# Performance work log

Hardware: AMD Instinct MI355X
Metric: run time of the kernel (lower is better)

## Reference

```python
import jax, jax.numpy as jnp
import numpy as np

WS = 7       # window_size
SHIFT = 3    # shift_size
NH = 4       # num_heads


def _layernorm(x, g, b, eps=1e-5):
    m = jnp.mean(x, axis=-1, keepdims=True)
    v = jnp.mean((x - m) ** 2, axis=-1, keepdims=True)
    return (x - m) * jax.lax.rsqrt(v + eps) * g + b


def _mha(x, wq, bq, wk, bk, wv, bv, wo, bo):
    # x: [n, s, c]; weights stored as [in, out]
    n, s, c = x.shape
    dk = c // NH
    q = (x @ wq + bq).reshape(n, s, NH, dk).transpose(0, 2, 1, 3)
    k = (x @ wk + bk).reshape(n, s, NH, dk).transpose(0, 2, 1, 3)
    v = (x @ wv + bv).reshape(n, s, NH, dk).transpose(0, 2, 1, 3)
    scores = jnp.einsum('nhqd,nhkd->nhqk', q, k) / jnp.sqrt(jnp.float32(dk))
    attn = jax.nn.softmax(scores, axis=-1)  # dropout is identity in eval
    out = jnp.einsum('nhqk,nhkd->nhqd', attn, v)
    out = out.transpose(0, 2, 1, 3).reshape(n, s, c)
    return out @ wo + bo


def _window_partition(x):
    B, H, W, C = x.shape
    x = x.reshape(B, H // WS, WS, W // WS, WS, C)
    x = x.transpose(0, 1, 3, 2, 4, 5)
    return x.reshape(-1, WS * WS, C)


def _window_reverse(wins, H, W):
    C = wins.shape[-1]
    B = wins.shape[0] // ((H // WS) * (W // WS))
    x = wins.reshape(B, H // WS, W // WS, WS, WS, C)
    x = x.transpose(0, 1, 3, 2, 4, 5)
    return x.reshape(B, H, W, C)


def setup_inputs() -> dict:
    key = jax.random.key(0)
    ks = jax.random.split(key, 16)
    C = 128
    def w(k, shape):
        return jax.random.normal(k, shape, dtype=jnp.float32) * 0.02
    return {
        'x':  jax.random.normal(ks[0], (4, 56, 56, C), dtype=jnp.float32),
        'wq': w(ks[1], (C, C)), 'bq': jnp.zeros((C,), jnp.float32),
        'wk': w(ks[2], (C, C)), 'bk': jnp.zeros((C,), jnp.float32),
        'wv': w(ks[3], (C, C)), 'bv': jnp.zeros((C,), jnp.float32),
        'wo': w(ks[4], (C, C)), 'bo': jnp.zeros((C,), jnp.float32),
        'w1': w(ks[5], (C, 4 * C)), 'b1': jnp.zeros((4 * C,), jnp.float32),
        'w2': w(ks[6], (4 * C, C)), 'b2': jnp.zeros((C,), jnp.float32),
        'g1': jnp.ones((C,), jnp.float32), 'be1': jnp.zeros((C,), jnp.float32),
        'g2': jnp.ones((C,), jnp.float32), 'be2': jnp.zeros((C,), jnp.float32),
    }


def reference(x, wq, bq, wk, bk, wv, bv, wo, bo, w1, b1, w2, b2, g1, be1, g2, be2):
    B, H, W, C = x.shape
    # cyclic shift
    xs = jnp.roll(x, shift=(-SHIFT, -SHIFT), axis=(1, 2)) if SHIFT > 0 else x
    # windowed attention (note: original code replaces x, no residual here)
    wins = _window_partition(xs)                         # [B*nW, 49, C]
    attn_wins = _mha(wins, wq, bq, wk, bk, wv, bv, wo, bo)
    xs = _window_reverse(attn_wins, H, W)
    x = jnp.roll(xs, shift=(SHIFT, SHIFT), axis=(1, 2)) if SHIFT > 0 else xs
    # global attention residual branch (flatten H*W tokens)
    xf = x.reshape(B, H * W, C)
    xf = xf + _mha(_layernorm(xf, g1, be1), wq, bq, wk, bk, wv, bv, wo, bo)
    # MLP residual branch
    h = jax.nn.gelu(_layernorm(xf, g2, be2) @ w1 + b1, approximate=False)
    xf = xf + (h @ w2 + b2)
    return xf.reshape(B, H, W, C)
```

## Files before the change

kernel.cpp:

```cpp
#include <hip/hip_runtime.h>
#include <hip/hip_bf16.h>
#include <math.h>

#define NH 4
#define DK 32
#define CC 128
#define HW 56
#define SHIFT 3
#define NTOK 12544
#define S_GLB 3136
#define VTW_STRIDE 12608
#define SCALE_L2E 0.25503488f

typedef unsigned short u16;
typedef short bf16x8 __attribute__((ext_vector_type(8)));
typedef unsigned short u16x8 __attribute__((ext_vector_type(8)));
typedef float f32x4 __attribute__((ext_vector_type(4)));

static __device__ __forceinline__ u16 f2bf(float f) {
  unsigned int b = __builtin_bit_cast(unsigned int, f);
  return (u16)((b + 0x7FFFu + ((b >> 16) & 1u)) >> 16);
}
static __device__ __forceinline__ unsigned pk2bf(float a, float b) {
  unsigned r;
  asm("v_cvt_pk_bf16_f32 %0, %1, %2" : "=v"(r) : "v"(a), "v"(b));
  return r;
}
static __device__ __forceinline__ float fexp2(float x) {
  float r;
  asm("v_exp_f32 %0, %1" : "=v"(r) : "v"(x));
  return r;
}
static __device__ __forceinline__ void gload16(const void* g, void* l) {
  __builtin_amdgcn_global_load_lds(
      (const __attribute__((address_space(1))) unsigned int*)g,
      (__attribute__((address_space(3))) unsigned int*)l, 16, 0, 0);
}

__global__ __launch_bounds__(256) void prep_k(
    const float* __restrict__ w1, const float* __restrict__ w2,
    const float* __restrict__ wq, const float* __restrict__ wk,
    const float* __restrict__ wv, const float* __restrict__ wo,
    const float* __restrict__ x,
    u16* __restrict__ w1t, u16* __restrict__ w2t,
    u16* __restrict__ wqkvt, u16* __restrict__ wot, u16* __restrict__ xg) {
  if (blockIdx.x < 768) {
    const int idx = blockIdx.x * 256 + threadIdx.x;
    if (idx < 65536) {
      const int c = idx >> 7, r = idx & 127;
      w1t[idx] = f2bf(w1[r * 512 + c]);
    } else if (idx < 131072) {
      const int o = idx - 65536;
      const int c = o / 512, r = o - c * 512;
      w2t[o] = f2bf(w2[r * 128 + c]);
    } else {
      const int o = idx - 131072;
      const int which = o >> 14, oo = o & 16383;
      const int c = oo >> 7, r = oo & 127;
      const float* src = (which == 0) ? wq : (which == 1) ? wk : (which == 2) ? wv : wo;
      u16* dst = (which < 3) ? (wqkvt + which * 16384) : wot;
      dst[oo] = f2bf(src[r * 128 + c]);
    }
  } else {
    const int bid = blockIdx.x - 768;
    const int t = bid * 2 + (threadIdx.x >> 7);
    const int c = threadIdx.x & 127;
    const int win = t / 49, tok = t % 49;
    const int b = win >> 6, wrem = win & 63;
    const int wi = wrem >> 3, wj = wrem & 7;
    const int i = tok / 7, j = tok % 7;
    int hh = wi * 7 + i + SHIFT; if (hh >= HW) hh -= HW;
    int ww = wj * 7 + j + SHIFT; if (ww >= HW) ww -= HW;
    xg[(size_t)t * CC + c] = f2bf(x[((size_t)(b * HW + hh) * HW + ww) * CC + c]);
  }
}

template <int PATH>
__global__ __launch_bounds__(256) void qkv_gemm_k(
    const u16* __restrict__ xin, const u16* __restrict__ wqkvt,
    const float* __restrict__ bq, const float* __restrict__ bk,
    const float* __restrict__ bv,
    u16* __restrict__ qo, u16* __restrict__ ko, u16* __restrict__ vto) {
  __shared__ __align__(16) u16 xs[64][136];
  __shared__ __align__(16) u16 wt[64][136];
  const int tid = threadIdx.x;
  const int w = tid >> 6, lane = tid & 63;
  const int lo = lane & 15, hi = lane >> 4, hi4 = hi * 4;
  const int m0 = blockIdx.x * 64;
  const int widx = blockIdx.y >> 1;
  const int n0 = (blockIdx.y & 1) * 64;
  {
    const int r = tid >> 2, sg = tid & 3;
    const u16* sx = &xin[(size_t)(m0 + r) * CC + sg * 32];
    const u16* sw = &wqkvt[(size_t)widx * CC * CC + (size_t)(n0 + r) * CC + sg * 32];
#pragma unroll
    for (int j = 0; j < 4; ++j) {
      *reinterpret_cast<u16x8*>(&xs[r][sg * 32 + j * 8]) = *reinterpret_cast<const u16x8*>(&sx[j * 8]);
      *reinterpret_cast<u16x8*>(&wt[r][sg * 32 + j * 8]) = *reinterpret_cast<const u16x8*>(&sw[j * 8]);
    }
  }
  __syncthreads();
  if (widx < 2) {
    const float* bias = (widx == 0) ? bq : bk;
    u16* outp = (widx == 0) ? qo : ko;
    const float oscale = (widx == 0) ? SCALE_L2E : 1.0f;
    f32x4 acc[4];
#pragma unroll
    for (int st = 0; st < 4; ++st) {
      const float b_ = bias[n0 + st * 16 + lo];
      acc[st] = (f32x4){b_, b_, b_, b_};
    }
#pragma unroll
    for (int kk = 0; kk < 4; ++kk) {
      const bf16x8 af = *reinterpret_cast<const bf16x8*>(&xs[w * 16 + lo][kk * 32 + 8 * hi]);
#pragma unroll
      for (int st = 0; st < 4; ++st) {
        const bf16x8 bfr = *reinterpret_cast<const bf16x8*>(&wt[st * 16 + lo][kk * 32 + 8 * hi]);
        acc[st] = __builtin_amdgcn_mfma_f32_16x16x32_bf16(af, bfr, acc[st], 0, 0, 0);
      }
    }
#pragma unroll
    for (int r = 0; r < 4; ++r) {
      const int mm = m0 + w * 16 + hi4 + r;
      size_t rowbase, hstride;
      if (PATH == 0) {
        const int win = mm / 49, tok = mm - win * 49;
        rowbase = ((size_t)(win * 4) * 49 + tok) * DK;
        hstride = (size_t)49 * DK;
      } else {
        const int b = mm / S_GLB, s = mm - b * S_GLB;
        rowbase = ((size_t)(b * 4) * S_GLB + s) * DK;
        hstride = (size_t)S_GLB * DK;
      }
#pragma unroll
      for (int st = 0; st < 4; ++st) {
        const int c = n0 + st * 16 + lo, h = c >> 5, d = c & 31;
        outp[rowbase + (size_t)h * hstride + d] = f2bf(acc[st][r] * oscale);
      }
    }
  } else {
    f32x4 bias4;
#pragma unroll
    for (int r = 0; r < 4; ++r) bias4[r] = bv[n0 + w * 16 + hi4 + r];
    f32x4 acc[4];
#pragma unroll
    for (int st = 0; st < 4; ++st) acc[st] = bias4;
#pragma unroll
    for (int kk = 0; kk < 4; ++kk) {
      const bf16x8 af = *reinterpret_cast<const bf16x8*>(&wt[w * 16 + lo][kk * 32 + 8 * hi]);
#pragma unroll
      for (int st = 0; st < 4; ++st) {
        const bf16x8 bfr = *reinterpret_cast<const bf16x8*>(&xs[st * 16 + lo][kk * 32 + 8 * hi]);
        acc[st] = __builtin_amdgcn_mfma_f32_16x16x32_bf16(af, bfr, acc[st], 0, 0, 0);
      }
    }
#pragma unroll
    for (int st = 0; st < 4; ++st) {
      const int mm = m0 + st * 16 + lo;
#pragma unroll
      for (int r = 0; r < 4; ++r) {
        const int c = n0 + w * 16 + hi4 + r;
        if (PATH == 0) {
          vto[(size_t)c * VTW_STRIDE + mm] = f2bf(acc[st][r]);
        } else {
          const int b = mm / S_GLB, s = mm - b * S_GLB;
          vto[((size_t)b * CC + c) * S_GLB + s] = f2bf(acc[st][r]);
        }
      }
    }
  }
}

__global__ __launch_bounds__(256) void win_attn_k(
    const u16* __restrict__ qw, const u16* __restrict__ kw,
    const u16* __restrict__ vtw, u16* __restrict__ aow) {
  __shared__ __align__(16) u16 psh[4][16][72];
  const int tid = threadIdx.x;
  const int wvi = tid >> 6, lane = tid & 63;
  const int lo = lane & 15, hi = lane >> 4, hi4 = hi * 4;
  const int wh = blockIdx.x * 4 + wvi;
  const int win = wh >> 2, hd = wh & 3;
  const f32x4 zero4 = {0.f, 0.f, 0.f, 0.f};
  bf16x8 ones;
#pragma unroll
  for (int j = 0; j < 8; ++j) ones[j] = (short)0x3F80;

  bf16x8 kf[4], vf[2][2];
#pragma unroll
  for (int st = 0; st < 4; ++st)
    kf[st] = *reinterpret_cast<const bf16x8*>(&kw[((size_t)wh * 49 + st * 16 + lo) * DK + 8 * hi]);
#pragma unroll
  for (int dst = 0; dst < 2; ++dst)
#pragma unroll
    for (int kch = 0; kch < 2; ++kch)
      vf[dst][kch] = *reinterpret_cast<const bf16x8*>(
          &vtw[(size_t)(hd * DK + dst * 16 + lo) * VTW_STRIDE + win * 49 + kch * 32 + 8 * hi]);

#pragma unroll
  for (int g = 0; g < 4; ++g) {
    const bf16x8 qf = *reinterpret_cast<const bf16x8*>(
        &qw[((size_t)wh * 49 + g * 16 + lo) * DK + 8 * hi]);
    f32x4 s4[4];
#pragma unroll
    for (int st = 0; st < 4; ++st) {
      s4[st] = __builtin_amdgcn_mfma_f32_16x16x32_bf16(kf[st], qf, zero4, 0, 0, 0);
#pragma unroll
      for (int r = 0; r < 4; ++r)
        if (st * 16 + hi4 + r >= 49) s4[st][r] = -1e30f;
    }
#pragma unroll
    for (int st = 0; st < 4; ++st) {
      uint2 pk;
      pk.x = pk2bf(fexp2(s4[st][0]), fexp2(s4[st][1]));
      pk.y = pk2bf(fexp2(s4[st][2]), fexp2(s4[st][3]));
      *reinterpret_cast<uint2*>(&psh[wvi][lo][st * 16 + hi4]) = pk;
    }
    asm volatile("" ::: "memory");
    f32x4 acc0 = zero4, acc1 = zero4, lacc = zero4;
#pragma unroll
    for (int kch = 0; kch < 2; ++kch) {
      const bf16x8 pa = *reinterpret_cast<const bf16x8*>(&psh[wvi][lo][kch * 32 + 8 * hi]);
      acc0 = __builtin_amdgcn_mfma_f32_16x16x32_bf16(pa, vf[0][kch], acc0, 0, 0, 0);
      acc1 = __builtin_amdgcn_mfma_f32_16x16x32_bf16(pa, vf[1][kch], acc1, 0, 0, 0);
      lacc = __builtin_amdgcn_mfma_f32_16x16x32_bf16(pa, ones, lacc, 0, 0, 0);
    }
#pragma unroll
    for (int r = 0; r < 4; ++r) {
      const int qrow = g * 16 + hi4 + r;
      if (qrow < 49) {
        const float rl = 1.0f / lacc[r];
        const size_t tw = (size_t)win * 49 + qrow;
        aow[tw * CC + hd * DK + lo] = f2bf(acc0[r] * rl);
        aow[tw * CC + hd * DK + 16 + lo] = f2bf(acc1[r] * rl);
      }
    }
  }
}

__global__ __launch_bounds__(256) void glb_attn_k(
    const u16* __restrict__ qg, const u16* __restrict__ kg,
    const u16* __restrict__ vtg, float* __restrict__ po, float* __restrict__ pl) {
  __shared__ __align__(16) u16 ksh[2][64][32];
  __shared__ __align__(16) u16 vtsh[2][32][64];
  __shared__ __align__(16) u16 psh[4][16][64];
  const int tid = threadIdx.x;
  const int w = tid >> 6, lane = tid & 63;
  const int lo = lane & 15, hi = lane >> 4, hi4 = hi * 4;
  const int bh = blockIdx.y;
  const int q0 = blockIdx.x * 64;
  const int sp = blockIdx.z;
  const int kt_beg = sp * 25;
  const int kt_end = sp ? 49 : 25;
  const f32x4 zero4 = {0.f, 0.f, 0.f, 0.f};
  bf16x8 ones;
#pragma unroll
  for (int j = 0; j < 8; ++j) ones[j] = (short)0x3F80;

  const bf16x8 qfrag = *reinterpret_cast<const bf16x8*>(
      &qg[((size_t)bh * S_GLB + q0 + w * 16 + lo) * DK + 8 * hi]);
  const u16* kg0 = kg + (size_t)bh * S_GLB * DK;
  const u16* vg0 = vtg + (size_t)bh * DK * S_GLB;

  const u16* ksrc = kg0 + (size_t)(w * 16 + (lane >> 2)) * DK + (lane & 3) * 8;
  const u16* vsrc = vg0 + (size_t)(w * 8 + (lane >> 3)) * S_GLB + ((lane & 7) ^ (lane >> 3)) * 8;
  u16* kdst0 = &ksh[0][w * 16][0]; u16* kdst1 = &ksh[1][w * 16][0];
  u16* vdst0 = &vtsh[0][w * 8][0]; u16* vdst1 = &vtsh[1][w * 8][0];

  f32x4 oacc0 = zero4, oacc1 = zero4, lacc = zero4;

  gload16(ksrc + (size_t)kt_beg * 64 * DK, kdst0);
  gload16(vsrc + (size_t)kt_beg * 64, vdst0);
  __syncthreads();

  char* const pbase = (char*)&psh[w][lo][0];
  char* const vbase0 = (char*)&vtsh[0][0][0];
  const unsigned swz = (unsigned)(lo & 7) << 4;

  for (int kt = kt_beg; kt < kt_end; ++kt) {
    const int cur = (kt - kt_beg) & 1;
    if (kt + 1 < kt_end) {
      gload16(ksrc + (size_t)(kt + 1) * 64 * DK, cur ? kdst0 : kdst1);
      gload16(vsrc + (size_t)(kt + 1) * 64, cur ? vdst0 : vdst1);
    }
    f32x4 s4[4];
#pragma unroll
    for (int st = 0; st < 4; ++st) {
      const bf16x8 kfrag = *reinterpret_cast<const bf16x8*>(&ksh[cur][st * 16 + lo][8 * hi]);
      s4[st] = __builtin_amdgcn_mfma_f32_16x16x32_bf16(kfrag, qfrag, zero4, 0, 0, 0);
    }
#pragma unroll
    for (int st = 0; st < 4; ++st) {
      uint2 pk;
      pk.x = pk2bf(fexp2(s4[st][0]), fexp2(s4[st][1]));
      pk.y = pk2bf(fexp2(s4[st][2]), fexp2(s4[st][3]));
      *reinterpret_cast<uint2*>(pbase + (((unsigned)(st * 32 + hi * 8)) ^ swz)) = pk;
    }
    asm volatile("" ::: "memory");
    char* const vrow0 = vbase0 + (size_t)cur * (32 * 64 * 2) + lo * 128;
#pragma unroll
    for (int kch = 0; kch < 2; ++kch) {
      const unsigned off = ((unsigned)(kch * 64 + hi * 16)) ^ swz;
      const bf16x8 pa = *reinterpret_cast<const bf16x8*>(pbase + off);
      const bf16x8 v0 = *reinterpret_cast<const bf16x8*>(vrow0 + off);
      const bf16x8 v1 = *reinterpret_cast<const bf16x8*>(vrow0 + 16 * 128 + off);
      oacc0 = __builtin_amdgcn_mfma_f32_16x16x32_bf16(pa, v0, oacc0, 0, 0, 0);
      oacc1 = __builtin_amdgcn_mfma_f32_16x16x32_bf16(pa, v1, oacc1, 0, 0, 0);
      lacc = __builtin_amdgcn_mfma_f32_16x16x32_bf16(pa, ones, lacc, 0, 0, 0);
    }
    __syncthreads();
  }

  const int b = bh >> 2, hd = bh & 3;
  float* pob = po + (size_t)sp * NTOK * CC;
#pragma unroll
  for (int r = 0; r < 4; ++r) {
    const size_t t = (size_t)b * S_GLB + q0 + w * 16 + hi4 + r;
    pob[t * CC + hd * DK + lo] = oacc0[r];
    pob[t * CC + hd * DK + 16 + lo] = oacc1[r];
    if (lo == 0)
      pl[((size_t)sp * 16 + bh) * S_GLB + q0 + w * 16 + hi4 + r] = lacc[r];
  }
}

template <int MODE>
__global__ __launch_bounds__(256) void proj_ln_k(
    const u16* __restrict__ ain, const float* __restrict__ po,
    const float* __restrict__ pl, const u16* __restrict__ wot,
    const float* __restrict__ bo, const float* __restrict__ resid,
    const float* __restrict__ lng, const float* __restrict__ lnb,
    float* __restrict__ xfo, u16* __restrict__ ybf) {
  __shared__ __align__(16) u16 xs[64][136];
  __shared__ __align__(16) u16 wt[128][136];
  const int tid = threadIdx.x;
  const int w = tid >> 6, lane = tid & 63;
  const int lo = lane & 15, hi = lane >> 4, hi4 = hi * 4;
  const int m0 = blockIdx.x * 64;
  {
    const int r = tid >> 2, sg = tid & 3;
    if (MODE == 0) {
      const u16* sx = &ain[(size_t)(m0 + r) * CC + sg * 32];
#pragma unroll
      for (int j = 0; j < 4; ++j)
        *reinterpret_cast<u16x8*>(&xs[r][sg * 32 + j * 8]) = *reinterpret_cast<const u16x8*>(&sx[j * 8]);
    } else {
      const int mm = m0 + r;
      const int b = mm / S_GLB, s_ = mm - b * S_GLB;
      const float l0 = pl[((size_t)(b * 4 + sg)) * S_GLB + s_];
      const float l1 = pl[((size_t)(16 + b * 4 + sg)) * S_GLB + s_];
      const float rl = 1.0f / (l0 + l1);
      const float* pa = &po[(size_t)mm * CC + sg * 32];
      const float* pb = pa + (size_t)NTOK * CC;
#pragma unroll
      for (int j = 0; j < 32; j += 4) {
        const float4 a4 = *reinterpret_cast<const float4*>(&pa[j]);
        const float4 b4 = *reinterpret_cast<const float4*>(&pb[j]);
        uint2 pk;
        pk.x = pk2bf((a4.x + b4.x) * rl, (a4.y + b4.y) * rl);
        pk.y = pk2bf((a4.z + b4.z) * rl, (a4.w + b4.w) * rl);
        *reinterpret_cast<uint2*>(&xs[r][sg * 32 + j]) = pk;
      }
    }
    const int r2 = tid >> 1, sg2 = tid & 1;
    const u16* sw = &wot[(size_t)r2 * CC + sg2 * 64];
#pragma unroll
    for (int j = 0; j < 8; ++j)
      *reinterpret_cast<u16x8*>(&wt[r2][sg2 * 64 + j * 8]) = *reinterpret_cast<const u16x8*>(&sw[j * 8]);
  }
  __syncthreads();
  f32x4 acc[8];
#pragma unroll
  for (int st = 0; st < 8; ++st) {
    const float b_ = bo[st * 16 + lo];
    acc[st] = (f32x4){b_, b_, b_, b_};
  }
#pragma unroll
  for (int kk = 0; kk < 4; ++kk) {
    const bf16x8 af = *reinterpret_cast<const bf16x8*>(&xs[w * 16 + lo][kk * 32 + 8 * hi]);
#pragma unroll
    for (int st = 0; st < 8; ++st) {
      const bf16x8 bfr = *reinterpret_cast<const bf16x8*>(&wt[st * 16 + lo][kk * 32 + 8 * hi]);
      acc[st] = __builtin_amdgcn_mfma_f32_16x16x32_bf16(af, bfr, acc[st], 0, 0, 0);
    }
  }
  float gv[8], bv2[8];
#pragma unroll
  for (int st = 0; st < 8; ++st) { gv[st] = lng[st * 16 + lo]; bv2[st] = lnb[st * 16 + lo]; }
#pragma unroll
  for (int r = 0; r < 4; ++r) {
    const int mm = m0 + w * 16 + hi4 + r;
    size_t trow;
    if (MODE == 0) {
      const int win = mm / 49, tok = mm - win * 49;
      const int b = win >> 6, wi = (win >> 3) & 7, wj = win & 7;
      const int ii = tok / 7, jj = tok - ii * 7;
      int hr = wi * 7 + ii + SHIFT; if (hr >= HW) hr -= HW;
      int wr = wj * 7 + jj + SHIFT; if (wr >= HW) wr -= HW;
      trow = (size_t)b * S_GLB + hr * HW + wr;
    } else {
      trow = (size_t)mm;
    }
    float v[8];
    float s = 0.f, sq = 0.f;
#pragma unroll
    for (int st = 0; st < 8; ++st) {
      float t_ = acc[st][r];
      if (MODE == 1) t_ += resid[trow * CC + st * 16 + lo];
      v[st] = t_;
      s += t_;
      sq += t_ * t_;
    }
    s += __shfl_xor(s, 1); s += __shfl_xor(s, 2); s += __shfl_xor(s, 4); s += __shfl_xor(s, 8);
    sq += __shfl_xor(sq, 1); sq += __shfl_xor(sq, 2); sq += __shfl_xor(sq, 4); sq += __shfl_xor(sq, 8);
    const float mu = s * 0.0078125f;
    const float rsig = rsqrtf(sq * 0.0078125f - mu * mu + 1e-5f);
#pragma unroll
    for (int st = 0; st < 8; ++st) {
      const size_t idx = trow * CC + st * 16 + lo;
      xfo[idx] = v[st];
      ybf[idx] = f2bf((v[st] - mu) * rsig * gv[st] + bv2[st]);
    }
  }
}

__global__ __launch_bounds__(256) void gemm1_k(
    const u16* __restrict__ ybf, const u16* __restrict__ w1t,
    const float* __restrict__ b1, u16* __restrict__ hb) {
  __shared__ __align__(16) u16 xs[64][136];
  __shared__ __align__(16) u16 wt[64][136];
  const int tid = threadIdx.x;
  const int w = tid >> 6, lane = tid & 63;
  const int lo = lane & 15, hi = lane >> 4;
  const int m0 = blockIdx.x * 64, n0 = blockIdx.y * 64;
  {
    const int r = tid >> 2, sg = tid & 3;
    const u16* src_x = &ybf[(size_t)(m0 + r) * CC + sg * 32];
    const u16* src_w = &w1t[(size_t)(n0 + r) * CC + sg * 32];
#pragma unroll
    for (int j = 0; j < 4; ++j) {
      *reinterpret_cast<u16x8*>(&xs[r][sg * 32 + j * 8]) = *reinterpret_cast<const u16x8*>(&src_x[j * 8]);
      *reinterpret_cast<u16x8*>(&wt[r][sg * 32 + j * 8]) = *reinterpret_cast<const u16x8*>(&src_w[j * 8]);
    }
  }
  __syncthreads();
  f32x4 acc[4];
#pragma unroll
  for (int st = 0; st < 4; ++st) {
    const float bv = b1[n0 + st * 16 + lo];
    acc[st] = (f32x4){bv, bv, bv, bv};
  }
#pragma unroll
  for (int kk = 0; kk < 4; ++kk) {
    const bf16x8 af = *reinterpret_cast<const bf16x8*>(&xs[w * 16 + lo][kk * 32 + 8 * hi]);
#pragma unroll
    for (int st = 0; st < 4; ++st) {
      const bf16x8 bfr = *reinterpret_cast<const bf16x8*>(&wt[st * 16 + lo][kk * 32 + 8 * hi]);
      acc[st] = __builtin_amdgcn_mfma_f32_16x16x32_bf16(af, bfr, acc[st], 0, 0, 0);
    }
  }
#pragma unroll
  for (int st = 0; st < 4; ++st) {
#pragma unroll
    for (int r = 0; r < 4; ++r) {
      const float val = acc[st][r];
      const float gel = 0.5f * val * (1.0f + erff(val * 0.70710678118f));
      hb[(size_t)(m0 + w * 16 + (hi << 2) + r) * 512 + n0 + st * 16 + lo] = f2bf(gel);
    }
  }
}

__global__ __launch_bounds__(256) void gemm2_k(
    const u16* __restrict__ hb, const u16* __restrict__ w2t,
    const float* __restrict__ b2, const float* __restrict__ xf,
    float* __restrict__ out) {
  __shared__ __align__(16) u16 xs[64][136];
  __shared__ __align__(16) u16 wt[64][136];
  const int tid = threadIdx.x;
  const int w = tid >> 6, lane = tid & 63;
  const int lo = lane & 15, hi = lane >> 4;
  const int m0 = blockIdx.x * 64, n0 = blockIdx.y * 64;
  f32x4 acc[4];
#pragma unroll
  for (int st = 0; st < 4; ++st) {
    const float bv = b2[n0 + st * 16 + lo];
    acc[st] = (f32x4){bv, bv, bv, bv};
  }
  for (int kc = 0; kc < 4; ++kc) {
    if (kc) __syncthreads();
    {
      const int r = tid >> 2, sg = tid & 3;
      const u16* src_x = &hb[(size_t)(m0 + r) * 512 + kc * 128 + sg * 32];
      const u16* src_w = &w2t[(size_t)(n0 + r) * 512 + kc * 128 + sg * 32];
#pragma unroll
      for (int j = 0; j < 4; ++j) {
        *reinterpret_cast<u16x8*>(&xs[r][sg * 32 + j * 8]) = *reinterpret_cast<const u16x8*>(&src_x[j * 8]);
        *reinterpret_cast<u16x8*>(&wt[r][sg * 32 + j * 8]) = *reinterpret_cast<const u16x8*>(&src_w[j * 8]);
      }
    }
    __syncthreads();
#pragma unroll
    for (int kk = 0; kk < 4; ++kk) {
      const bf16x8 af = *reinterpret_cast<const bf16x8*>(&xs[w * 16 + lo][kk * 32 + 8 * hi]);
#pragma unroll
      for (int st = 0; st < 4; ++st) {
        const bf16x8 bfr = *reinterpret_cast<const bf16x8*>(&wt[st * 16 + lo][kk * 32 + 8 * hi]);
        acc[st] = __builtin_amdgcn_mfma_f32_16x16x32_bf16(af, bfr, acc[st], 0, 0, 0);
      }
    }
  }
#pragma unroll
  for (int st = 0; st < 4; ++st) {
#pragma unroll
    for (int r = 0; r < 4; ++r) {
      const size_t idx = (size_t)(m0 + w * 16 + (hi << 2) + r) * CC + n0 + st * 16 + lo;
      out[idx] = xf[idx] + acc[st][r];
    }
  }
}

extern "C" void kernel_launch(void* const* d_in, const int* in_sizes, int n_in,
                              void* d_out, int out_size, void* d_ws, size_t ws_size,
                              hipStream_t stream) {
  (void)in_sizes; (void)n_in; (void)out_size; (void)ws_size;
  const float* x   = (const float*)d_in[0];
  const float* wq  = (const float*)d_in[1];
  const float* bq  = (const float*)d_in[2];
  const float* wk  = (const float*)d_in[3];
  const float* bk  = (const float*)d_in[4];
  const float* wv  = (const float*)d_in[5];
  const float* bv  = (const float*)d_in[6];
  const float* wo  = (const float*)d_in[7];
  const float* bo  = (const float*)d_in[8];
  const float* w1  = (const float*)d_in[9];
  const float* b1  = (const float*)d_in[10];
  const float* w2  = (const float*)d_in[11];
  const float* b2  = (const float*)d_in[12];
  const float* g1  = (const float*)d_in[13];
  const float* be1 = (const float*)d_in[14];
  const float* g2  = (const float*)d_in[15];
  const float* be2 = (const float*)d_in[16];
  float* out = (float*)d_out;

  char* p = (char*)d_ws;
  auto alloc = [&](size_t bytes) { char* r = p; p += (bytes + 255) & ~(size_t)255; return r; };
  float* xf  = (float*)alloc((size_t)NTOK * CC * 4);
  u16* xg    = (u16*)alloc((size_t)NTOK * CC * 2);
  u16* qw    = (u16*)alloc((size_t)NTOK * CC * 2 + 4096);
  u16* kw    = (u16*)alloc((size_t)NTOK * CC * 2 + 4096);
  u16* vtw   = (u16*)alloc((size_t)CC * VTW_STRIDE * 2);
  u16* aow   = (u16*)alloc((size_t)NTOK * CC * 2);
  u16* hb    = (u16*)alloc((size_t)NTOK * 512 * 2);
  float* po  = (float*)alloc((size_t)2 * NTOK * CC * 4);
  float* pl  = (float*)alloc((size_t)2 * 16 * S_GLB * 4);
  u16* wqkvt = (u16*)alloc(3 * 16384 * 2);
  u16* wot   = (u16*)alloc(16384 * 2);
  u16* w1t   = (u16*)alloc(65536 * 2);
  u16* w2t   = (u16*)alloc(65536 * 2);

  prep_k<<<768 + NTOK / 2, 256, 0, stream>>>(
      w1, w2, wq, wk, wv, wo, x, w1t, w2t, wqkvt, wot, xg);
  qkv_gemm_k<0><<<dim3(NTOK / 64, 6), 256, 0, stream>>>(xg, wqkvt, bq, bk, bv, qw, kw, vtw);
  win_attn_k<<<256, 256, 0, stream>>>(qw, kw, vtw, aow);
  proj_ln_k<0><<<NTOK / 64, 256, 0, stream>>>(
      aow, nullptr, nullptr, wot, bo, nullptr, g1, be1, xf, xg);
  qkv_gemm_k<1><<<dim3(NTOK / 64, 6), 256, 0, stream>>>(xg, wqkvt, bq, bk, bv, qw, kw, vtw);
  glb_attn_k<<<dim3(S_GLB / 64, 16, 2), 256, 0, stream>>>(qw, kw, vtw, po, pl);
  proj_ln_k<1><<<NTOK / 64, 256, 0, stream>>>(
      nullptr, po, pl, wot, bo, xf, g2, be2, xf, xg);
  gemm1_k<<<dim3(NTOK / 64, 8), 256, 0, stream>>>(xg, w1t, b1, hb);
  gemm2_k<<<dim3(NTOK / 64, 2), 256, 0, stream>>>(hb, w2t, b2, xf, out);
}
```

Baseline: 111.4 us.

## Triple-buffer global attention K/V loads and remap blocks for XCD locality

The global attention kernel moves from double to triple buffering of K and V tiles in shared memory. Explicit vmcnt waits and a single barrier per iteration replace the trailing __syncthreads, so loads run two tiles ahead. The 3D grid is flattened into a 1D grid with a swizzled block index, so that blocks sharing the same head and split land on the same XCD and reuse K/V in L2. This costs extra LDS, which may lower occupancy, and the hand-managed waitcnt ordering is fragile.

Measured after the change: 118.0 us. 5.9% more time.

```diff
diff --git a/kernel.cpp b/kernel.cpp
--- a/kernel.cpp
+++ b/kernel.cpp
@@ -240,17 +240,20 @@
 __global__ __launch_bounds__(256) void glb_attn_k(
     const u16* __restrict__ qg, const u16* __restrict__ kg,
     const u16* __restrict__ vtg, float* __restrict__ po, float* __restrict__ pl) {
-  __shared__ __align__(16) u16 ksh[2][64][32];
-  __shared__ __align__(16) u16 vtsh[2][32][64];
+  __shared__ __align__(16) u16 ksh[3][64][32];
+  __shared__ __align__(16) u16 vtsh[3][32][64];
   __shared__ __align__(16) u16 psh[4][16][64];
   const int tid = threadIdx.x;
   const int w = tid >> 6, lane = tid & 63;
   const int lo = lane & 15, hi = lane >> 4, hi4 = hi * 4;
-  const int bh = blockIdx.y;
-  const int q0 = blockIdx.x * 64;
-  const int sp = blockIdx.z;
-  const int kt_beg = sp * 25;
-  const int kt_end = sp ? 49 : 25;
+  const int wg = blockIdx.x;
+  const int sid = (wg & 7) * 196 + (wg >> 3);
+  const int sp = sid / 784;
+  const int rem = sid - sp * 784;
+  const int bh = rem / 49;
+  const int q0 = (rem - bh * 49) * 64;
+  const int kt0 = sp * 25;
+  const int nt = sp ? 24 : 25;
   const f32x4 zero4 = {0.f, 0.f, 0.f, 0.f};
   bf16x8 ones;
 #pragma unroll
@@ -261,26 +264,32 @@
   const u16* kg0 = kg + (size_t)bh * S_GLB * DK;
   const u16* vg0 = vtg + (size_t)bh * DK * S_GLB;
 
-  const u16* ksrc = kg0 + (size_t)(w * 16 + (lane >> 2)) * DK + (lane & 3) * 8;
-  const u16* vsrc = vg0 + (size_t)(w * 8 + (lane >> 3)) * S_GLB + ((lane & 7) ^ (lane >> 3)) * 8;
-  u16* kdst0 = &ksh[0][w * 16][0]; u16* kdst1 = &ksh[1][w * 16][0];
-  u16* vdst0 = &vtsh[0][w * 8][0]; u16* vdst1 = &vtsh[1][w * 8][0];
+  const u16* ksrc = kg0 + (size_t)(w * 16 + (lane >> 2)) * DK + (lane & 3) * 8
+                    + (size_t)kt0 * 64 * DK;
+  const u16* vsrc = vg0 + (size_t)(w * 8 + (lane >> 3)) * S_GLB + ((lane & 7) ^ (lane >> 3)) * 8
+                    + (size_t)kt0 * 64;
+  u16* const kdst = &ksh[0][w * 16][0];
+  u16* const vdst = &vtsh[0][w * 8][0];
 
   f32x4 oacc0 = zero4, oacc1 = zero4, lacc = zero4;
 
-  gload16(ksrc + (size_t)kt_beg * 64 * DK, kdst0);
-  gload16(vsrc + (size_t)kt_beg * 64, vdst0);
-  __syncthreads();
+  gload16(ksrc, kdst);
+  gload16(vsrc, vdst);
+  gload16(ksrc + (size_t)64 * DK, kdst + 64 * 32);
+  gload16(vsrc + 64, vdst + 32 * 64);
 
   char* const pbase = (char*)&psh[w][lo][0];
-  char* const vbase0 = (char*)&vtsh[0][0][0];
   const unsigned swz = (unsigned)(lo & 7) << 4;
 
-  for (int kt = kt_beg; kt < kt_end; ++kt) {
-    const int cur = (kt - kt_beg) & 1;
-    if (kt + 1 < kt_end) {
-      gload16(ksrc + (size_t)(kt + 1) * 64 * DK, cur ? kdst0 : kdst1);
-      gload16(vsrc + (size_t)(kt + 1) * 64, cur ? vdst0 : vdst1);
+  int cur = 0, nxt = 2;
+  for (int i = 0; i < nt; ++i) {
+    if (i == nt - 1) { asm volatile("s_waitcnt vmcnt(0)" ::: "memory"); }
+    else             { asm volatile("s_waitcnt vmcnt(2)" ::: "memory"); }
+    __builtin_amdgcn_sched_barrier(0);
+    __builtin_amdgcn_s_barrier();
+    if (i + 2 < nt) {
+      gload16(ksrc + (size_t)(i + 2) * 64 * DK, kdst + nxt * 64 * 32);
+      gload16(vsrc + (size_t)(i + 2) * 64, vdst + nxt * 32 * 64);
     }
     f32x4 s4[4];
 #pragma unroll
@@ -296,7 +305,7 @@
       *reinterpret_cast<uint2*>(pbase + (((unsigned)(st * 32 + hi * 8)) ^ swz)) = pk;
     }
     asm volatile("" ::: "memory");
-    char* const vrow0 = vbase0 + (size_t)cur * (32 * 64 * 2) + lo * 128;
+    char* const vrow0 = (char*)&vtsh[cur][0][0] + lo * 128;
 #pragma unroll
     for (int kch = 0; kch < 2; ++kch) {
       const unsigned off = ((unsigned)(kch * 64 + hi * 16)) ^ swz;
@@ -307,7 +316,8 @@
       oacc1 = __builtin_amdgcn_mfma_f32_16x16x32_bf16(pa, v1, oacc1, 0, 0, 0);
       lacc = __builtin_amdgcn_mfma_f32_16x16x32_bf16(pa, ones, lacc, 0, 0, 0);
     }
-    __syncthreads();
+    cur = (cur == 2) ? 0 : cur + 1;
+    nxt = (nxt == 2) ? 0 : nxt + 1;
   }
 
   const int b = bh >> 2, hd = bh & 3;
@@ -563,7 +573,7 @@
   proj_ln_k<0><<<NTOK / 64, 256, 0, stream>>>(
       aow, nullptr, nullptr, wot, bo, nullptr, g1, be1, xf, xg);
   qkv_gemm_k<1><<<dim3(NTOK / 64, 6), 256, 0, stream>>>(xg, wqkvt, bq, bk, bv, qw, kw, vtw);
-  glb_attn_k<<<dim3(S_GLB / 64, 16, 2), 256, 0, stream>>>(qw, kw, vtw, po, pl);
+  glb_attn_k<<<1568, 256, 0, stream>>>(qw, kw, vtw, po, pl);
   proj_ln_k<1><<<NTOK / 64, 256, 0, stream>>>(
       nullptr, po, pl, wot, bo, xf, g2, be2, xf, xg);
   gemm1_k<<<dim3(NTOK / 64, 8), 256, 0, stream>>>(xg, w1t, b1, hb);
```
